# Kernel optimization log

Measured on AMD Instinct MI355X. Metric: run time of the kernel, lower is better.

The kernel has to match this reference:

```python
import jax, jax.numpy as jnp
import numpy as np

BLOCK = 128          # fp8 quantization block size (from linear_deepseek_v3)
FP8_MAX = 448.0      # max representable value of float8_e4m3fn
F8 = jnp.float8_e4m3fn
G, T, K, N = 8, 1024, 7168, 2048


def setup_inputs() -> dict:
    key = jax.random.key(0)
    kx, kw, kb = jax.random.split(key, 3)
    xs = jax.random.normal(kx, (G, T, K), jnp.float32)
    # Build an fp8 block-quantized weight + per-(128x128)-block fp32 scale,
    # matching the stored self.weight (fp8) and self.scale parameters.
    w_raw = jax.random.normal(kw, (G, N, K), jnp.float32)
    wb = w_raw.reshape(G, N // BLOCK, BLOCK, K // BLOCK, BLOCK)
    amax = jnp.max(jnp.abs(wb), axis=(2, 4))            # [G, NB, KB]
    scale = amax / FP8_MAX
    w_q = (wb / scale[:, :, None, :, None]).astype(F8).astype(jnp.float32)
    weight = w_q.reshape(G, N, K)                        # fp8 code values held in fp32
    bias = jax.random.normal(kb, (G, N), jnp.float32) * 0.02
    return {"xs": xs, "weight": weight, "scale": scale, "bias": bias}


def reference(xs, weight, scale, bias):
    """Grouped fp8 block-quantized GEMM with inline dequant.
    xs:     [G, T, K] fp32 activations (one slab per group)
    weight: [G, N, K] fp8-quantized weights (stored as fp32 code values)
    scale:  [G, N/128, K/128] fp32 per-block weight scales
    bias:   [G, N] fp32
    """
    g, t, k = xs.shape
    n = weight.shape[1]
    kb, nb = k // BLOCK, n // BLOCK
    # --- act_quant_deepseek_v3: per (token, 128-col block) absmax/448 scale ---
    xb = xs.reshape(g, t, kb, BLOCK)
    a_scale = jnp.max(jnp.abs(xb), axis=-1) / FP8_MAX        # [G, T, KB]
    x_q = (xb / a_scale[..., None]).astype(F8).astype(jnp.float32)
    x_deq = (x_q * a_scale[..., None]).reshape(g, t, k)      # fused dequant
    # --- weight dequant: broadcast per-(128x128)-block scale ---
    w_deq = (weight.reshape(g, nb, BLOCK, kb, BLOCK)
             * scale[:, :, None, :, None]).reshape(g, n, k)
    # --- grouped GEMM (y = x A^T) + bias, fp32 accumulation ---
    y = jnp.einsum('gtk,gnk->gtn', x_deq, w_deq) + bias[:, None, :]
    return y
```

## Files before the change

kernel.cpp:

```cpp
#include <hip/hip_runtime.h>
#include <hip/hip_bf16.h>
#include <stdint.h>

#define G_ 8
#define T_ 1024
#define K_ 7168
#define N_ 2048
#define KB_ (K_/128)
#define NB_ (N_/128)
#define NT_ (K_/64)

typedef __attribute__((ext_vector_type(4))) float f32x4;
typedef __attribute__((ext_vector_type(2))) float f32x2;
typedef __attribute__((ext_vector_type(8))) short bf16x8;

typedef __attribute__((address_space(3))) uint32_t lds_u32_t;
typedef const __attribute__((address_space(1))) uint32_t gbl_u32_t;

__device__ __forceinline__ void gload_lds16(const void* gsrc, const void* ldst)
{
    __builtin_amdgcn_global_load_lds(
        (gbl_u32_t*)(uintptr_t)gsrc,
        (lds_u32_t*)(uint32_t)(uintptr_t)ldst, 16, 0, 0);
}

__device__ __forceinline__ void blockbar()
{
    asm volatile("" ::: "memory");
    __builtin_amdgcn_s_barrier();
    asm volatile("" ::: "memory");
}

__global__ __launch_bounds__(256) void act_quant_kernel(
    const float* __restrict__ xs, __hip_bfloat16* __restrict__ xq)
{
    const int grp = (blockIdx.x * 256 + threadIdx.x) >> 5;
    const int l   = threadIdx.x & 31;
    const size_t base = (size_t)grp * 128 + (size_t)l * 4;

    const float4 v = *(const float4*)(xs + base);
    float am = fmaxf(fmaxf(fabsf(v.x), fabsf(v.y)), fmaxf(fabsf(v.z), fabsf(v.w)));
#pragma unroll
    for (int off = 1; off <= 16; off <<= 1)
        am = fmaxf(am, __shfl_xor(am, off, 64));
    const float s = am / 448.0f;

    const int pk01 = __builtin_amdgcn_cvt_pk_fp8_f32(v.x / s, v.y / s, 0, false);
    const int pk23 = __builtin_amdgcn_cvt_pk_fp8_f32(v.z / s, v.w / s, 0, false);
    const f32x2 d01 = __builtin_amdgcn_cvt_pk_f32_fp8(pk01, false);
    const f32x2 d23 = __builtin_amdgcn_cvt_pk_f32_fp8(pk23, false);

    union { uint2 u; __hip_bfloat16 h[4]; } p;
    p.h[0] = __float2bfloat16(d01[0] * s);
    p.h[1] = __float2bfloat16(d01[1] * s);
    p.h[2] = __float2bfloat16(d23[0] * s);
    p.h[3] = __float2bfloat16(d23[1] * s);
    *(uint2*)(xq + base) = p.u;
}

__global__ __launch_bounds__(256) void wdeq_kernel(
    const float* __restrict__ w, const float* __restrict__ scale,
    __hip_bfloat16* __restrict__ wq)
{
    const size_t i8 = ((size_t)blockIdx.x * 256 + threadIdx.x) * 8;
    const int k   = (int)(i8 % K_);
    const int row = (int)(i8 / K_);
    const int g   = row >> 11;
    const int n   = row & (N_ - 1);
    const float s = scale[((size_t)g * NB_ + (n >> 7)) * KB_ + (k >> 7)];
    const float4 a = *(const float4*)(w + i8);
    const float4 b = *(const float4*)(w + i8 + 4);
    union { uint4 u; __hip_bfloat16 h[8]; } p;
    p.h[0] = __float2bfloat16(a.x * s);
    p.h[1] = __float2bfloat16(a.y * s);
    p.h[2] = __float2bfloat16(a.z * s);
    p.h[3] = __float2bfloat16(a.w * s);
    p.h[4] = __float2bfloat16(b.x * s);
    p.h[5] = __float2bfloat16(b.y * s);
    p.h[6] = __float2bfloat16(b.z * s);
    p.h[7] = __float2bfloat16(b.w * s);
    *(uint4*)(wq + i8) = p.u;
}

#define MFMA_Q(MH, NH)                                                        \
  { _Pragma("unroll") for (int m = 0; m < 4; ++m) {                           \
      _Pragma("unroll") for (int n = 0; n < 2; ++n) {                         \
        _Pragma("unroll") for (int ks = 0; ks < 2; ++ks) {                    \
          acc[(MH)*4+m][(NH)*2+n] = __builtin_amdgcn_mfma_f32_16x16x32_bf16(  \
              bA[m*2+ks], bB[((NH)*2+n)*2+ks], acc[(MH)*4+m][(NH)*2+n],       \
              0, 0, 0);                                                       \
  } } } }

#define LDA(m, ks, MH, b)                                                     \
  bA[(m)*2+(ks)] = *(const bf16x8*)(smem + (b)*32768 +                        \
      (wrow + (MH)*64 + (m)*16 + l15)*128 + colK[ks])

#define LDB(n, ks, b)                                                         \
  bB[(n)*2+(ks)] = *(const bf16x8*)(smem + 65536 + (b)*32768 +                \
      (wcol + (n)*16 + l15)*128 + colK[ks])

#define STG_A(c, t, b) gload_lds16(pA[c] + (size_t)(t)*64,                    \
      smem + (b)*32768 + (c)*8192 + dstw)
#define STG_B(c, t, b) gload_lds16(pB[c] + (size_t)(t)*64,                    \
      smem + 65536 + (b)*32768 + (c)*8192 + dstw)

__global__ __launch_bounds__(512) void gemm8_kernel(
    const __hip_bfloat16* __restrict__ xq, const __hip_bfloat16* __restrict__ wq,
    const float* __restrict__ bias, float* __restrict__ y)
{
    __shared__ char smem[131072];

    const int bx0 = blockIdx.x;
    const int bx  = (bx0 & 7) * 32 + (bx0 >> 3);
    const int g   = bx >> 5;
    const int tm  = (bx >> 3) & 3;
    const int tn  = bx & 7;
    const int t0  = tm * 256, n0 = tn * 256;

    const int tid = threadIdx.x, lane = tid & 63, wid = tid >> 6;
    const int l15 = lane & 15, lhi = lane >> 4;
    const int wrow = (wid >> 2) * 128;
    const int wcol = (wid & 3) * 64;

    const __hip_bfloat16* Ag = xq + (size_t)g * T_ * K_;
    const __hip_bfloat16* Bg = wq + (size_t)g * N_ * K_;

    const int srow = tid >> 3;
    const int xoff = ((tid & 7) ^ (srow & 7)) * 8;
    const __hip_bfloat16* pA[4];
    const __hip_bfloat16* pB[4];
#pragma unroll
    for (int c = 0; c < 4; ++c) {
        pA[c] = Ag + (size_t)(t0 + c * 64 + srow) * K_ + xoff;
        pB[c] = Bg + (size_t)(n0 + c * 64 + srow) * K_ + xoff;
    }
    const int dstw = wid * 1024;

    const int rxor = (l15 & 7) << 4;
    int colK[2];
    colK[0] = (lhi * 16) ^ rxor;
    colK[1] = (64 + lhi * 16) ^ rxor;

    f32x4 acc[8][4] = {};
    bf16x8 bA[8], bB[8];

#pragma unroll
    for (int c = 0; c < 4; ++c) STG_A(c, 0, 0);
#pragma unroll
    for (int c = 0; c < 4; ++c) STG_B(c, 0, 0);
#pragma unroll
    for (int c = 0; c < 4; ++c) STG_A(c, 1, 1);
#pragma unroll
    for (int c = 0; c < 4; ++c) STG_B(c, 1, 1);
    asm volatile("s_waitcnt vmcnt(8)" ::: "memory");
    blockbar();

    for (int u = 0; u < NT_; ++u) {
        const int cb = u & 1;
        const bool pf = (u + 2 < NT_);

        LDA(0,0,0,cb); LDA(0,1,0,cb); LDA(1,0,0,cb); LDA(1,1,0,cb);
        LDA(2,0,0,cb); LDA(2,1,0,cb); LDA(3,0,0,cb); LDA(3,1,0,cb);
        LDB(0,0,cb);   LDB(0,1,cb);   LDB(1,0,cb);   LDB(1,1,cb);
        blockbar();
        asm volatile("s_waitcnt lgkmcnt(0)" ::: "memory");
        __builtin_amdgcn_s_setprio(1);
        MFMA_Q(0, 0);
        __builtin_amdgcn_s_setprio(0);
        blockbar();

        LDB(2,0,cb); LDB(2,1,cb); LDB(3,0,cb); LDB(3,1,cb);
        if (pf) { STG_A(0, u+2, cb); STG_A(2, u+2, cb); }
        blockbar();
        asm volatile("s_waitcnt lgkmcnt(0)" ::: "memory");
        __builtin_amdgcn_s_setprio(1);
        MFMA_Q(0, 1);
        __builtin_amdgcn_s_setprio(0);
        blockbar();

        LDA(0,0,1,cb); LDA(0,1,1,cb); LDA(1,0,1,cb); LDA(1,1,1,cb);
        LDA(2,0,1,cb); LDA(2,1,1,cb); LDA(3,0,1,cb); LDA(3,1,1,cb);
        if (pf) { STG_B(0, u+2, cb); STG_B(1, u+2, cb); }
        blockbar();
        asm volatile("s_waitcnt lgkmcnt(0)" ::: "memory");
        __builtin_amdgcn_s_setprio(1);
        MFMA_Q(1, 0);
        __builtin_amdgcn_s_setprio(0);
        blockbar();

        if (pf) { STG_B(2, u+2, cb); STG_B(3, u+2, cb);
                  STG_A(1, u+2, cb); STG_A(3, u+2, cb); }
        blockbar();
        __builtin_amdgcn_s_setprio(1);
        MFMA_Q(1, 1);
        __builtin_amdgcn_s_setprio(0);
        if (pf)                 asm volatile("s_waitcnt vmcnt(8)" ::: "memory");
        else if (u + 1 < NT_)   asm volatile("s_waitcnt vmcnt(0)" ::: "memory");
        blockbar();
    }

    float* Yg = y + (size_t)g * T_ * N_;
#pragma unroll
    for (int n = 0; n < 4; ++n) {
        const int col = n0 + wcol + n * 16 + l15;
        const float bv = bias[g * N_ + col];
#pragma unroll
        for (int m = 0; m < 8; ++m) {
            const int r0 = t0 + wrow + m * 16 + lhi * 4;
#pragma unroll
            for (int j = 0; j < 4; ++j)
                Yg[(size_t)(r0 + j) * N_ + col] = acc[m][n][j] + bv;
        }
    }
}

__global__ __launch_bounds__(256) void gemm_kernel(
    const __hip_bfloat16* __restrict__ xq, const float* __restrict__ w,
    const float* __restrict__ scale, const float* __restrict__ bias,
    float* __restrict__ y)
{
    __shared__ __hip_bfloat16 As[128][64];
    __shared__ __hip_bfloat16 Bs[128][64];

    const int bx = blockIdx.x;
    const int g  = bx >> 7;
    const int tm = (bx >> 4) & 7;
    const int tn = bx & 15;
    const int t0 = tm * 128;
    const int n0 = tn * 128;

    const int tid  = threadIdx.x;
    const int lane = tid & 63;
    const int wid  = tid >> 6;

    const __hip_bfloat16* Ag = xq + (size_t)g * T_ * K_;
    const float*          Wg = w  + (size_t)g * N_ * K_;

    const int arow = tid >> 3;
    const int acol = (tid & 7) * 8;
    const int brow0 = tid >> 4;
    const int bcol  = (tid & 15) * 4;

    const int wr  = (wid >> 1) * 64;
    const int wc  = (wid & 1) * 64;
    const int l15 = lane & 15;
    const int lhi = lane >> 4;

    f32x4 acc[4][4] = {};

    for (int kt = 0; kt < K_ / 64; ++kt) {
        const int k0 = kt * 64;
#pragma unroll
        for (int j = 0; j < 4; ++j) {
            const __hip_bfloat16* src =
                Ag + (size_t)(t0 + j * 32 + arow) * K_ + k0 + acol;
            gload_lds16(src, (char*)(&As[0][0]) + j * 4096 + wid * 1024);
        }
        const float svw = scale[((size_t)g * NB_ + tn) * KB_ + (kt >> 1)];
#pragma unroll
        for (int i = 0; i < 8; ++i) {
            const int r = i * 16 + brow0;
            const float4 wv = *(const float4*)(Wg + (size_t)(n0 + r) * K_ + k0 + bcol);
            union { uint2 u; __hip_bfloat16 h[4]; } p;
            p.h[0] = __float2bfloat16(wv.x * svw);
            p.h[1] = __float2bfloat16(wv.y * svw);
            p.h[2] = __float2bfloat16(wv.z * svw);
            p.h[3] = __float2bfloat16(wv.w * svw);
            *(uint2*)(&Bs[r][bcol]) = p.u;
        }
        __syncthreads();
#pragma unroll
        for (int kk = 0; kk < 64; kk += 32) {
            bf16x8 av[4], bv[4];
#pragma unroll
            for (int m = 0; m < 4; ++m)
                av[m] = *(const bf16x8*)&As[wr + m * 16 + l15][kk + lhi * 8];
#pragma unroll
            for (int n = 0; n < 4; ++n)
                bv[n] = *(const bf16x8*)&Bs[wc + n * 16 + l15][kk + lhi * 8];
#pragma unroll
            for (int m = 0; m < 4; ++m)
#pragma unroll
                for (int n = 0; n < 4; ++n)
                    acc[m][n] = __builtin_amdgcn_mfma_f32_16x16x32_bf16(
                        av[m], bv[n], acc[m][n], 0, 0, 0);
        }
        __syncthreads();
    }

    float* Yg = y + (size_t)g * T_ * N_;
#pragma unroll
    for (int n = 0; n < 4; ++n) {
        const int col = n0 + wc + n * 16 + l15;
        const float bv = bias[g * N_ + col];
#pragma unroll
        for (int m = 0; m < 4; ++m) {
            const int row0 = t0 + wr + m * 16 + lhi * 4;
#pragma unroll
            for (int j = 0; j < 4; ++j)
                Yg[(size_t)(row0 + j) * N_ + col] = acc[m][n][j] + bv;
        }
    }
}

extern "C" void kernel_launch(void* const* d_in, const int* in_sizes, int n_in,
                              void* d_out, int out_size, void* d_ws, size_t ws_size,
                              hipStream_t stream)
{
    const float* xs     = (const float*)d_in[0];
    const float* weight = (const float*)d_in[1];
    const float* scale  = (const float*)d_in[2];
    const float* bias   = (const float*)d_in[3];
    float* y = (float*)d_out;

    __hip_bfloat16* xq = (__hip_bfloat16*)d_ws;
    const size_t xq_bytes = (size_t)G_ * T_ * K_ * 2;
    const size_t wq_bytes = (size_t)G_ * N_ * K_ * 2;

    act_quant_kernel<<<(G_ * T_ * KB_) / 8, 256, 0, stream>>>(xs, xq);

    if (ws_size >= xq_bytes + wq_bytes) {
        __hip_bfloat16* wq = (__hip_bfloat16*)((char*)d_ws + xq_bytes);
        wdeq_kernel<<<(int)(((size_t)G_ * N_ * K_ / 8) / 256), 256, 0, stream>>>(
            weight, scale, wq);
        gemm8_kernel<<<256, 512, 0, stream>>>(xq, wq, bias, y);
    } else {
        gemm_kernel<<<G_ * (T_ / 128) * (N_ / 128), 256, 0, stream>>>(
            xq, weight, scale, bias, y);
    }
}
```

Measured before the change: 383.6 us.

## Fuse weight dequant into 256x256 GEMM mainloop via register-staged fp32 loads

```diff
diff --git a/kernel.cpp b/kernel.cpp
--- a/kernel.cpp
+++ b/kernel.cpp
@@ -56,30 +56,6 @@
     p.h[2] = __float2bfloat16(d23[0] * s);
     p.h[3] = __float2bfloat16(d23[1] * s);
     *(uint2*)(xq + base) = p.u;
-}
-
-__global__ __launch_bounds__(256) void wdeq_kernel(
-    const float* __restrict__ w, const float* __restrict__ scale,
-    __hip_bfloat16* __restrict__ wq)
-{
-    const size_t i8 = ((size_t)blockIdx.x * 256 + threadIdx.x) * 8;
-    const int k   = (int)(i8 % K_);
-    const int row = (int)(i8 / K_);
-    const int g   = row >> 11;
-    const int n   = row & (N_ - 1);
-    const float s = scale[((size_t)g * NB_ + (n >> 7)) * KB_ + (k >> 7)];
-    const float4 a = *(const float4*)(w + i8);
-    const float4 b = *(const float4*)(w + i8 + 4);
-    union { uint4 u; __hip_bfloat16 h[8]; } p;
-    p.h[0] = __float2bfloat16(a.x * s);
-    p.h[1] = __float2bfloat16(a.y * s);
-    p.h[2] = __float2bfloat16(a.z * s);
-    p.h[3] = __float2bfloat16(a.w * s);
-    p.h[4] = __float2bfloat16(b.x * s);
-    p.h[5] = __float2bfloat16(b.y * s);
-    p.h[6] = __float2bfloat16(b.z * s);
-    p.h[7] = __float2bfloat16(b.w * s);
-    *(uint4*)(wq + i8) = p.u;
 }
 
 #define MFMA_Q(MH, NH)                                                        \
@@ -101,12 +77,32 @@
 
 #define STG_A(c, t, b) gload_lds16(pA[c] + (size_t)(t)*64,                    \
       smem + (b)*32768 + (c)*8192 + dstw)
-#define STG_B(c, t, b) gload_lds16(pB[c] + (size_t)(t)*64,                    \
-      smem + 65536 + (b)*32768 + (c)*8192 + dstw)
+
+#define LOAD_B(t)                                                             \
+  { _Pragma("unroll") for (int c = 0; c < 4; ++c) {                           \
+      const float* s_ = pW[c] + (size_t)(t) * 64;                             \
+      br[c*2]   = *(const f32x4*)(s_);                                        \
+      br[c*2+1] = *(const f32x4*)(s_ + 4);                                    \
+  } }
+
+#define WRITE_B(t, b)                                                         \
+  { const int kb_ = (t) >> 1;                                                 \
+    const float s0_ = scale[scb + kb_];                                       \
+    const float s1_ = scale[scb + KB_ + kb_];                                 \
+    _Pragma("unroll") for (int c = 0; c < 4; ++c) {                           \
+      const float sc_ = (c < 2) ? s0_ : s1_;                                  \
+      union { __hip_bfloat16 h[8]; bf16x8 v; } u_;                            \
+      _Pragma("unroll") for (int e = 0; e < 4; ++e) {                         \
+        u_.h[e]     = __float2bfloat16(br[c*2][e]   * sc_);                   \
+        u_.h[e + 4] = __float2bfloat16(br[c*2+1][e] * sc_);                   \
+      }                                                                       \
+      *(bf16x8*)(smem + 65536 + (b)*32768 + (c*64 + brow)*128 + bslot) = u_.v;\
+  } }
 
 __global__ __launch_bounds__(512) void gemm8_kernel(
-    const __hip_bfloat16* __restrict__ xq, const __hip_bfloat16* __restrict__ wq,
-    const float* __restrict__ bias, float* __restrict__ y)
+    const __hip_bfloat16* __restrict__ xq, const float* __restrict__ w,
+    const float* __restrict__ scale, const float* __restrict__ bias,
+    float* __restrict__ y)
 {
     __shared__ char smem[131072];
 
@@ -123,18 +119,24 @@
     const int wcol = (wid & 3) * 64;
 
     const __hip_bfloat16* Ag = xq + (size_t)g * T_ * K_;
-    const __hip_bfloat16* Bg = wq + (size_t)g * N_ * K_;
+    const float*          Wg = w  + (size_t)g * N_ * K_;
 
     const int srow = tid >> 3;
     const int xoff = ((tid & 7) ^ (srow & 7)) * 8;
     const __hip_bfloat16* pA[4];
-    const __hip_bfloat16* pB[4];
-#pragma unroll
-    for (int c = 0; c < 4; ++c) {
+#pragma unroll
+    for (int c = 0; c < 4; ++c)
         pA[c] = Ag + (size_t)(t0 + c * 64 + srow) * K_ + xoff;
-        pB[c] = Bg + (size_t)(n0 + c * 64 + srow) * K_ + xoff;
-    }
     const int dstw = wid * 1024;
+
+    const int brow  = tid >> 3;
+    const int gslot = tid & 7;
+    const int bslot = (gslot ^ (brow & 7)) * 16;
+    const float* pW[4];
+#pragma unroll
+    for (int c = 0; c < 4; ++c)
+        pW[c] = Wg + (size_t)(n0 + c * 64 + brow) * K_ + gslot * 8;
+    const int scb = ((size_t)g * NB_ + tn * 2) * KB_;
 
     const int rxor = (l15 & 7) << 4;
     int colK[2];
@@ -143,22 +145,26 @@
 
     f32x4 acc[8][4] = {};
     bf16x8 bA[8], bB[8];
-
+    f32x4 br[8];
+
+    LOAD_B(0);
 #pragma unroll
     for (int c = 0; c < 4; ++c) STG_A(c, 0, 0);
-#pragma unroll
-    for (int c = 0; c < 4; ++c) STG_B(c, 0, 0);
+    asm volatile("s_waitcnt vmcnt(4)" ::: "memory");
+    WRITE_B(0, 0);
+    LOAD_B(1);
 #pragma unroll
     for (int c = 0; c < 4; ++c) STG_A(c, 1, 1);
-#pragma unroll
-    for (int c = 0; c < 4; ++c) STG_B(c, 1, 1);
-    asm volatile("s_waitcnt vmcnt(8)" ::: "memory");
+    asm volatile("s_waitcnt vmcnt(4)" ::: "memory");
+    WRITE_B(1, 1);
+    asm volatile("s_waitcnt vmcnt(0) lgkmcnt(0)" ::: "memory");
     blockbar();
 
     for (int u = 0; u < NT_; ++u) {
         const int cb = u & 1;
         const bool pf = (u + 2 < NT_);
 
+        if (pf) LOAD_B(u + 2);
         LDA(0,0,0,cb); LDA(0,1,0,cb); LDA(1,0,0,cb); LDA(1,1,0,cb);
         LDA(2,0,0,cb); LDA(2,1,0,cb); LDA(3,0,0,cb); LDA(3,1,0,cb);
         LDB(0,0,cb);   LDB(0,1,cb);   LDB(1,0,cb);   LDB(1,1,cb);
@@ -180,7 +186,7 @@
 
         LDA(0,0,1,cb); LDA(0,1,1,cb); LDA(1,0,1,cb); LDA(1,1,1,cb);
         LDA(2,0,1,cb); LDA(2,1,1,cb); LDA(3,0,1,cb); LDA(3,1,1,cb);
-        if (pf) { STG_B(0, u+2, cb); STG_B(1, u+2, cb); }
+        if (pf) { STG_A(1, u+2, cb); STG_A(3, u+2, cb); }
         blockbar();
         asm volatile("s_waitcnt lgkmcnt(0)" ::: "memory");
         __builtin_amdgcn_s_setprio(1);
@@ -188,14 +194,15 @@
         __builtin_amdgcn_s_setprio(0);
         blockbar();
 
-        if (pf) { STG_B(2, u+2, cb); STG_B(3, u+2, cb);
-                  STG_A(1, u+2, cb); STG_A(3, u+2, cb); }
-        blockbar();
+        if (pf) {
+            asm volatile("s_waitcnt vmcnt(4)" ::: "memory");
+            WRITE_B(u + 2, cb);
+        } else if (u + 1 < NT_) {
+            asm volatile("s_waitcnt vmcnt(0)" ::: "memory");
+        }
         __builtin_amdgcn_s_setprio(1);
         MFMA_Q(1, 1);
         __builtin_amdgcn_s_setprio(0);
-        if (pf)                 asm volatile("s_waitcnt vmcnt(8)" ::: "memory");
-        else if (u + 1 < NT_)   asm volatile("s_waitcnt vmcnt(0)" ::: "memory");
         blockbar();
     }
 
@@ -210,95 +217,6 @@
 #pragma unroll
             for (int j = 0; j < 4; ++j)
                 Yg[(size_t)(r0 + j) * N_ + col] = acc[m][n][j] + bv;
-        }
-    }
-}
-
-__global__ __launch_bounds__(256) void gemm_kernel(
-    const __hip_bfloat16* __restrict__ xq, const float* __restrict__ w,
-    const float* __restrict__ scale, const float* __restrict__ bias,
-    float* __restrict__ y)
-{
-    __shared__ __hip_bfloat16 As[128][64];
-    __shared__ __hip_bfloat16 Bs[128][64];
-
-    const int bx = blockIdx.x;
-    const int g  = bx >> 7;
-    const int tm = (bx >> 4) & 7;
-    const int tn = bx & 15;
-    const int t0 = tm * 128;
-    const int n0 = tn * 128;
-
-    const int tid  = threadIdx.x;
-    const int lane = tid & 63;
-    const int wid  = tid >> 6;
-
-    const __hip_bfloat16* Ag = xq + (size_t)g * T_ * K_;
-    const float*          Wg = w  + (size_t)g * N_ * K_;
-
-    const int arow = tid >> 3;
-    const int acol = (tid & 7) * 8;
-    const int brow0 = tid >> 4;
-    const int bcol  = (tid & 15) * 4;
-
-    const int wr  = (wid >> 1) * 64;
-    const int wc  = (wid & 1) * 64;
-    const int l15 = lane & 15;
-    const int lhi = lane >> 4;
-
-    f32x4 acc[4][4] = {};
-
-    for (int kt = 0; kt < K_ / 64; ++kt) {
-        const int k0 = kt * 64;
-#pragma unroll
-        for (int j = 0; j < 4; ++j) {
-            const __hip_bfloat16* src =
-                Ag + (size_t)(t0 + j * 32 + arow) * K_ + k0 + acol;
-            gload_lds16(src, (char*)(&As[0][0]) + j * 4096 + wid * 1024);
-        }
-        const float svw = scale[((size_t)g * NB_ + tn) * KB_ + (kt >> 1)];
-#pragma unroll
-        for (int i = 0; i < 8; ++i) {
-            const int r = i * 16 + brow0;
-            const float4 wv = *(const float4*)(Wg + (size_t)(n0 + r) * K_ + k0 + bcol);
-            union { uint2 u; __hip_bfloat16 h[4]; } p;
-            p.h[0] = __float2bfloat16(wv.x * svw);
-            p.h[1] = __float2bfloat16(wv.y * svw);
-            p.h[2] = __float2bfloat16(wv.z * svw);
-            p.h[3] = __float2bfloat16(wv.w * svw);
-            *(uint2*)(&Bs[r][bcol]) = p.u;
-        }
-        __syncthreads();
-#pragma unroll
-        for (int kk = 0; kk < 64; kk += 32) {
-            bf16x8 av[4], bv[4];
-#pragma unroll
-            for (int m = 0; m < 4; ++m)
-                av[m] = *(const bf16x8*)&As[wr + m * 16 + l15][kk + lhi * 8];
-#pragma unroll
-            for (int n = 0; n < 4; ++n)
-                bv[n] = *(const bf16x8*)&Bs[wc + n * 16 + l15][kk + lhi * 8];
-#pragma unroll
-            for (int m = 0; m < 4; ++m)
-#pragma unroll
-                for (int n = 0; n < 4; ++n)
-                    acc[m][n] = __builtin_amdgcn_mfma_f32_16x16x32_bf16(
-                        av[m], bv[n], acc[m][n], 0, 0, 0);
-        }
-        __syncthreads();
-    }
-
-    float* Yg = y + (size_t)g * T_ * N_;
-#pragma unroll
-    for (int n = 0; n < 4; ++n) {
-        const int col = n0 + wc + n * 16 + l15;
-        const float bv = bias[g * N_ + col];
-#pragma unroll
-        for (int m = 0; m < 4; ++m) {
-            const int row0 = t0 + wr + m * 16 + lhi * 4;
-#pragma unroll
-            for (int j = 0; j < 4; ++j)
-                Yg[(size_t)(row0 + j) * N_ + col] = acc[m][n][j] + bv;
         }
     }
 }
@@ -314,18 +232,7 @@
     float* y = (float*)d_out;
 
     __hip_bfloat16* xq = (__hip_bfloat16*)d_ws;
-    const size_t xq_bytes = (size_t)G_ * T_ * K_ * 2;
-    const size_t wq_bytes = (size_t)G_ * N_ * K_ * 2;
 
     act_quant_kernel<<<(G_ * T_ * KB_) / 8, 256, 0, stream>>>(xs, xq);
-
-    if (ws_size >= xq_bytes + wq_bytes) {
-        __hip_bfloat16* wq = (__hip_bfloat16*)((char*)d_ws + xq_bytes);
-        wdeq_kernel<<<(int)(((size_t)G_ * N_ * K_ / 8) / 256), 256, 0, stream>>>(
-            weight, scale, wq);
-        gemm8_kernel<<<256, 512, 0, stream>>>(xq, wq, bias, y);
-    } else {
-        gemm_kernel<<<G_ * (T_ / 128) * (N_ / 128), 256, 0, stream>>>(
-            xq, weight, scale, bias, y);
-    }
-}
+    gemm8_kernel<<<256, 512, 0, stream>>>(xq, weight, scale, bias, y);
+}
```

Measured after the change: 385.1 us. No clear change (+0.4%).
